# Optimization experiments

Measured on AMD Instinct MI355X. Metric: run time of the kernel, lower is better.

## Reference

```python
import jax, jax.numpy as jnp
import numpy as np

DIM = 1024
NUM_HEADS = 16
HEAD_DIM = DIM // NUM_HEADS

def setup_inputs() -> dict:
    key = jax.random.key(0)
    ks = jax.random.split(key, 5)
    s = 1.0 / np.sqrt(DIM)
    x = jax.random.normal(ks[0], (2, 2048, DIM), dtype=jnp.float32)
    W_qkv = jax.random.uniform(ks[1], (DIM, 3 * DIM), dtype=jnp.float32, minval=-s, maxval=s)
    b_qkv = jax.random.uniform(ks[2], (3 * DIM,), dtype=jnp.float32, minval=-s, maxval=s)
    W_out = jax.random.uniform(ks[3], (DIM, DIM), dtype=jnp.float32, minval=-s, maxval=s)
    b_out = jax.random.uniform(ks[4], (DIM,), dtype=jnp.float32, minval=-s, maxval=s)
    return {"x": x, "W_qkv": W_qkv, "b_qkv": b_qkv, "W_out": W_out, "b_out": b_out}

def reference(x, W_qkv, b_qkv, W_out, b_out):
    B, S, _ = x.shape
    qkv = x @ W_qkv + b_qkv                       # [B,S,3*dim]
    q, k, v = jnp.split(qkv, 3, axis=-1)
    # [B,S,dim] -> [B,H,S,hd]
    def to_heads(t):
        return t.reshape(B, S, NUM_HEADS, HEAD_DIM).transpose(0, 2, 1, 3)
    q, k, v = to_heads(q), to_heads(k), to_heads(v)
    scale = HEAD_DIM ** -0.5
    scores = jnp.einsum('bhqd,bhkd->bhqk', q, k) * scale
    attn = jax.nn.softmax(scores, axis=-1)
    out = jnp.einsum('bhqk,bhkd->bhqd', attn, v)  # [B,H,S,hd]
    out = out.transpose(0, 2, 1, 3).reshape(B, S, DIM)
    return out @ W_out + b_out
```

## Files before the change

### kernel.cpp

```cpp
#include <hip/hip_runtime.h>
#include <math.h>

#define DIMM    1024
#define NHEADS  16
#define HDIM    64
#define BATCH   2
#define SEQ     2048
#define ROWS    (BATCH*SEQ)

typedef _Float16 f16x8 __attribute__((ext_vector_type(8)));
typedef _Float16 f16x4 __attribute__((ext_vector_type(4)));
typedef float    f32x4 __attribute__((ext_vector_type(4)));
typedef float    f32x16 __attribute__((ext_vector_type(16)));

__device__ inline void gl_lds16(const void* g, void* l) {
    __builtin_amdgcn_global_load_lds(
        (const __attribute__((address_space(1))) void*)g,
        (__attribute__((address_space(3))) void*)l, 16, 0, 0);
}

static __device__ inline unsigned packh(_Float16 a, _Float16 b) {
    unsigned short ua = __builtin_bit_cast(unsigned short, a);
    unsigned short ub = __builtin_bit_cast(unsigned short, b);
    return (unsigned)ua | ((unsigned)ub << 16);
}
static __device__ inline f16x8 mkfrag(unsigned a, unsigned b, unsigned c, unsigned d) {
    union { unsigned u[4]; f16x8 v; } x;
    x.u[0] = a; x.u[1] = b; x.u[2] = c; x.u[3] = d;
    return x.v;
}

__device__ void tcvt64(const float* __restrict__ in, _Float16* __restrict__ out,
                       int K, int N, int k0, int n0, float (*tile)[65], int t)
{
    {
        const int c4 = (t & 15) * 4;
        const int r  = t >> 4;
        #pragma unroll
        for (int i = 0; i < 4; i++) {
            const int rr = r + 16 * i;
            float4 v = *(const float4*)(in + (size_t)(k0 + rr) * N + n0 + c4);
            tile[rr][c4] = v.x; tile[rr][c4 + 1] = v.y;
            tile[rr][c4 + 2] = v.z; tile[rr][c4 + 3] = v.w;
        }
    }
    __syncthreads();
    #pragma unroll
    for (int i = 0; i < 2; i++) {
        const int seg = t + 256 * i;
        const int n   = seg >> 3;
        const int kc  = (seg & 7) * 8;
        f16x8 o;
        #pragma unroll
        for (int j = 0; j < 8; j++) o[j] = (_Float16)tile[kc + j][n];
        *(f16x8*)(out + (size_t)(n0 + n) * K + k0 + kc) = o;
    }
}

__global__ __launch_bounds__(256)
void prep_kernel(const float* __restrict__ x, const float* __restrict__ Wqkv,
                 const float* __restrict__ Wout, _Float16* __restrict__ xh,
                 _Float16* __restrict__ wqkvt, _Float16* __restrict__ woutt)
{
    __shared__ float tile[64][65];
    const int bx = blockIdx.x;
    const int t  = threadIdx.x;
    if (bx < 2048) {
        const int i = bx * 256 + t;
        const float4 a = *(const float4*)(x + (size_t)i * 8);
        const float4 b = *(const float4*)(x + (size_t)i * 8 + 4);
        f16x8 o;
        o[0] = (_Float16)a.x; o[1] = (_Float16)a.y; o[2] = (_Float16)a.z; o[3] = (_Float16)a.w;
        o[4] = (_Float16)b.x; o[5] = (_Float16)b.y; o[6] = (_Float16)b.z; o[7] = (_Float16)b.w;
        *(f16x8*)(xh + (size_t)i * 8) = o;
    } else if (bx < 2816) {
        const int id = bx - 2048;
        const int gx = id % 48, gy = id / 48;
        tcvt64(Wqkv, wqkvt, DIMM, 3 * DIMM, gy * 64, gx * 64, tile, t);
    } else {
        const int id = bx - 2816;
        const int gx = id & 15, gy = id >> 4;
        tcvt64(Wout, woutt, DIMM, DIMM, gy * 64, gx * 64, tile, t);
    }
}

__global__ __launch_bounds__(256)
void vtranspose_kernel(const _Float16* __restrict__ qkvh, _Float16* __restrict__ vt)
{
    __shared__ _Float16 tile[64][72];
    const int kt = blockIdx.x;
    const int bh = blockIdx.y;
    const int b  = bh >> 4, h = bh & 15;
    const int t  = threadIdx.x;
    {
        const int key = t >> 2, c4 = (t & 3) * 16;
        const _Float16* src = qkvh + ((size_t)(b * SEQ + kt * 64 + key)) * (3 * DIMM)
                              + 2 * DIMM + h * HDIM + c4;
        f16x8 v0 = *(const f16x8*)src;
        f16x8 v1 = *(const f16x8*)(src + 8);
        #pragma unroll
        for (int j = 0; j < 8; j++) {
            tile[c4 + j][key]     = v0[j];
            tile[c4 + 8 + j][key] = v1[j];
        }
    }
    __syncthreads();
    {
        const int d = t >> 2, k4 = (t & 3) * 16;
        f16x8 o0, o1;
        #pragma unroll
        for (int j = 0; j < 8; j++) { o0[j] = tile[d][k4 + j]; o1[j] = tile[d][k4 + 8 + j]; }
        _Float16* dst = vt + ((size_t)bh * 64 + d) * SEQ + kt * 64 + k4;
        *(f16x8*)dst       = o0;
        *(f16x8*)(dst + 8) = o1;
    }
}

template<int OUT_F16, int BM>
__global__ __launch_bounds__(256)
void hgemm_db_kernel(const _Float16* __restrict__ A, const _Float16* __restrict__ Bt,
                     const float* __restrict__ bias, void* __restrict__ Cout,
                     int N, int K)
{
    constexpr int MI = BM / 32;
    __shared__ _Float16 As[2][BM * 64];
    __shared__ _Float16 Bs[2][128 * 64];

    const int t    = threadIdx.x;
    const int w    = t >> 6, lane = t & 63;
    const int quad = lane >> 4, l16 = lane & 15;
    const int wr   = w >> 1, wc = w & 1;
    const int row0 = blockIdx.y * BM, col0 = blockIdx.x * 128;
    const int sw   = l16 & 7;

    f32x4 acc[MI][4];
    #pragma unroll
    for (int i = 0; i < MI; i++)
        #pragma unroll
        for (int j = 0; j < 4; j++)
            #pragma unroll
            for (int r = 0; r < 4; r++) acc[i][j][r] = 0.f;

    const _Float16* gA[MI];
    int aofs[MI];
    #pragma unroll
    for (int j = 0; j < MI; j++) {
        const int s   = t + 256 * j;
        const int row = s >> 3;
        const int kb  = (s & 7) ^ (row & 7);
        gA[j] = A + (size_t)(row0 + row) * K + kb * 8;
        aofs[j] = s * 8;
    }
    const _Float16* gB[4];
    int bofs[4];
    #pragma unroll
    for (int j = 0; j < 4; j++) {
        const int s   = t + 256 * j;
        const int row = s >> 3;
        const int kb  = (s & 7) ^ (row & 7);
        gB[j] = Bt + (size_t)(col0 + row) * K + kb * 8;
        bofs[j] = s * 8;
    }

    #pragma unroll
    for (int j = 0; j < MI; j++) gl_lds16(gA[j], &As[0][aofs[j]]);
    #pragma unroll
    for (int j = 0; j < 4; j++)  gl_lds16(gB[j], &Bs[0][bofs[j]]);
    #pragma unroll
    for (int j = 0; j < MI; j++) gA[j] += 64;
    #pragma unroll
    for (int j = 0; j < 4; j++)  gB[j] += 64;

    const int niter = K >> 6;
    #pragma unroll 1
    for (int it = 0; it < niter; it++) {
        const int cur = it & 1;
        __syncthreads();

        if (it + 1 < niter) {
            const int nxt = cur ^ 1;
            #pragma unroll
            for (int j = 0; j < MI; j++) gl_lds16(gA[j], &As[nxt][aofs[j]]);
            #pragma unroll
            for (int j = 0; j < 4; j++)  gl_lds16(gB[j], &Bs[nxt][bofs[j]]);
            #pragma unroll
            for (int j = 0; j < MI; j++) gA[j] += 64;
            #pragma unroll
            for (int j = 0; j < 4; j++)  gB[j] += 64;
        }

        const _Float16* AsC = &As[cur][0];
        const _Float16* BsC = &Bs[cur][0];
        f16x8 af[MI][2], bf[4][2];
        #pragma unroll
        for (int i = 0; i < MI; i++) {
            const int arow = wr * (BM / 2) + i * 16 + l16;
            #pragma unroll
            for (int hh = 0; hh < 2; hh++)
                af[i][hh] = *(const f16x8*)(AsC + (arow * 8 + ((hh * 4 + quad) ^ sw)) * 8);
        }
        #pragma unroll
        for (int j = 0; j < 4; j++) {
            const int brow = wc * 64 + j * 16 + l16;
            #pragma unroll
            for (int hh = 0; hh < 2; hh++)
                bf[j][hh] = *(const f16x8*)(BsC + (brow * 8 + ((hh * 4 + quad) ^ sw)) * 8);
        }
        #pragma unroll
        for (int i = 0; i < MI; i++)
            #pragma unroll
            for (int j = 0; j < 4; j++) {
                acc[i][j] = __builtin_amdgcn_mfma_f32_16x16x32_f16(af[i][0], bf[j][0], acc[i][j], 0, 0, 0);
                acc[i][j] = __builtin_amdgcn_mfma_f32_16x16x32_f16(af[i][1], bf[j][1], acc[i][j], 0, 0, 0);
            }
    }

    #pragma unroll
    for (int j = 0; j < 4; j++) {
        const int col = col0 + wc * 64 + j * 16 + l16;
        const float bv = bias[col];
        #pragma unroll
        for (int i = 0; i < MI; i++) {
            const int row = row0 + wr * (BM / 2) + i * 16 + quad * 4;
            #pragma unroll
            for (int r = 0; r < 4; r++) {
                const float v = acc[i][j][r] + bv;
                if (OUT_F16)
                    ((_Float16*)Cout)[(size_t)(row + r) * N + col] = (_Float16)v;
                else
                    ((float*)Cout)[(size_t)(row + r) * N + col] = v;
            }
        }
    }
}

__global__ __launch_bounds__(256, 4)
void flash_attn_kernel(const _Float16* __restrict__ qkv,
                       const _Float16* __restrict__ vtg,
                       _Float16* __restrict__ out)
{
    const int qt = blockIdx.x;
    const int bh = blockIdx.y;
    const int b  = bh >> 4, hd = bh & 15;
    const int t    = threadIdx.x;
    const int w    = t >> 6;
    const int lane = t & 63;
    const int qg   = w >> 1;
    const int kh   = w & 1;
    const int l31  = lane & 31;
    const int hf   = lane >> 5;
    const int l7   = lane & 7;

    __shared__ __align__(16) _Float16 Ks [2][64 * 64];
    __shared__ __align__(16) _Float16 Vts[2][64 * 64];

    const int q0 = qt * 64;
    const size_t rstr = 3 * DIMM;
    const _Float16* qbase = qkv + (size_t)b * SEQ * rstr;

    f16x8 qf[4];
    {
        const _Float16* qrow = qbase + (size_t)(q0 + qg * 32 + l31) * rstr + hd * HDIM;
        #pragma unroll
        for (int dd = 0; dd < 4; dd++)
            qf[dd] = *(const f16x8*)(qrow + dd * 16 + hf * 8);
    }

    f32x16 Oacc[2];
    #pragma unroll
    for (int dh = 0; dh < 2; dh++)
        #pragma unroll
        for (int r = 0; r < 16; r++) Oacc[dh][r] = 0.f;
    float lrow = 0.f;

    const int seg0 = t, seg1 = t + 256;
    const int r0 = seg0 >> 3, lb0 = (seg0 & 7) ^ (r0 & 7);
    const int r1 = seg1 >> 3, lb1 = (seg1 & 7) ^ (r1 & 7);
    const _Float16* gK0 = qbase + (size_t)r0 * rstr + DIMM + hd * HDIM + lb0 * 8;
    const _Float16* gK1 = qbase + (size_t)r1 * rstr + DIMM + hd * HDIM + lb1 * 8;
    const _Float16* gV0 = vtg + ((size_t)bh * 64 + r0) * SEQ + lb0 * 8;
    const _Float16* gV1 = vtg + ((size_t)bh * 64 + r1) * SEQ + lb1 * 8;

    gl_lds16(gK0, &Ks [0][seg0 * 8]);
    gl_lds16(gK1, &Ks [0][seg1 * 8]);
    gl_lds16(gV0, &Vts[0][seg0 * 8]);
    gl_lds16(gV1, &Vts[0][seg1 * 8]);

    #pragma unroll 2
    for (int k0 = 0; k0 < SEQ; k0 += 64) {
        const int cur = (k0 >> 6) & 1;
        const _Float16* KsC  = &Ks [cur][0];
        const _Float16* VtsC = &Vts[cur][0];

        __syncthreads();

        f32x16 sacc;
        #pragma unroll
        for (int r = 0; r < 16; r++) sacc[r] = 0.f;
        #pragma unroll
        for (int dd = 0; dd < 4; dd++) {
            f16x8 kf = *(const f16x8*)(KsC + (kh * 32 + l31) * 64 + (((dd * 2 + hf) ^ l7) * 8));
            sacc = __builtin_amdgcn_mfma_f32_32x32x16_f16(kf, qf[dd], sacc, 0, 0, 0);
        }

        if (k0 + 64 < SEQ) {
            const int nxt = cur ^ 1;
            gl_lds16(gK0 + (size_t)(k0 + 64) * rstr, &Ks [nxt][seg0 * 8]);
            gl_lds16(gK1 + (size_t)(k0 + 64) * rstr, &Ks [nxt][seg1 * 8]);
            gl_lds16(gV0 + (k0 + 64),                &Vts[nxt][seg0 * 8]);
            gl_lds16(gV1 + (k0 + 64),                &Vts[nxt][seg1 * 8]);
        }

        _Float16 hh[16];
        #pragma unroll
        for (int r = 0; r < 16; r++) {
            const float e = __expf(sacc[r] * 0.125f);
            hh[r] = (_Float16)e;
            lrow += (float)hh[r];
        }

        unsigned w01 = packh(hh[0],  hh[1]),  w23 = packh(hh[2],  hh[3]);
        unsigned w45 = packh(hh[4],  hh[5]),  w67 = packh(hh[6],  hh[7]);
        unsigned w89 = packh(hh[8],  hh[9]),  wab = packh(hh[10], hh[11]);
        unsigned wcd = packh(hh[12], hh[13]), wef = packh(hh[14], hh[15]);
        unsigned o01 = __shfl_xor((int)w01, 32), o23 = __shfl_xor((int)w23, 32);
        unsigned o45 = __shfl_xor((int)w45, 32), o67 = __shfl_xor((int)w67, 32);
        unsigned o89 = __shfl_xor((int)w89, 32), oab = __shfl_xor((int)wab, 32);
        unsigned ocd = __shfl_xor((int)wcd, 32), oef = __shfl_xor((int)wef, 32);
        f16x8 pa0 = mkfrag(hf ? o45 : w01, hf ? o67 : w23,
                           hf ? w45 : o01, hf ? w67 : o23);
        f16x8 pa1 = mkfrag(hf ? ocd : w89, hf ? oef : wab,
                           hf ? wcd : o89, hf ? wef : oab);

        #pragma unroll
        for (int dh = 0; dh < 2; dh++) {
            const _Float16* vrow = VtsC + (dh * 32 + l31) * 64;
            f16x8 vf0 = *(const f16x8*)(vrow + (((kh * 4 + 0 + hf) ^ l7) * 8));
            f16x8 vf1 = *(const f16x8*)(vrow + (((kh * 4 + 2 + hf) ^ l7) * 8));
            Oacc[dh] = __builtin_amdgcn_mfma_f32_32x32x16_f16(pa0, vf0, Oacc[dh], 0, 0, 0);
            Oacc[dh] = __builtin_amdgcn_mfma_f32_32x32x16_f16(pa1, vf1, Oacc[dh], 0, 0, 0);
        }
    }

    float lsum = lrow + __shfl_xor(lrow, 32);
    __syncthreads();
    float* Obuf = (float*)&Ks[0][0];
    float* lbuf = (float*)&Vts[0][0];
    if (kh) {
        #pragma unroll
        for (int dh = 0; dh < 2; dh++)
            #pragma unroll
            for (int r = 0; r < 16; r++) {
                const int q = (r & 3) + 8 * (r >> 2) + 4 * hf;
                Obuf[(qg * 32 + q) * 64 + dh * 32 + l31] = Oacc[dh][r];
            }
        if (lane < 32) lbuf[qg * 32 + lane] = lsum;
    }
    __syncthreads();
    if (!kh) {
        const float dnrec = 1.f / (lsum + lbuf[qg * 32 + l31]);
        float dq[16];
        #pragma unroll
        for (int r = 0; r < 16; r++)
            dq[r] = __shfl(dnrec, (r & 3) + 8 * (r >> 2) + 4 * hf);
        #pragma unroll
        for (int dh = 0; dh < 2; dh++)
            #pragma unroll
            for (int r = 0; r < 16; r++) {
                const int q = (r & 3) + 8 * (r >> 2) + 4 * hf;
                const float v = (Oacc[dh][r] + Obuf[(qg * 32 + q) * 64 + dh * 32 + l31])
                                * dq[r];
                out[(size_t)(b * SEQ + q0 + qg * 32 + q) * DIMM + hd * HDIM + dh * 32 + l31] =
                    (_Float16)v;
            }
    }
}

extern "C" void kernel_launch(void* const* d_in, const int* in_sizes, int n_in,
                              void* d_out, int out_size, void* d_ws, size_t ws_size,
                              hipStream_t stream)
{
    const float* x    = (const float*)d_in[0];
    const float* Wqkv = (const float*)d_in[1];
    const float* bqkv = (const float*)d_in[2];
    const float* Wout = (const float*)d_in[3];
    const float* bout = (const float*)d_in[4];
    float* out = (float*)d_out;

    _Float16* qkvh  = (_Float16*)d_ws;
    _Float16* attnh = qkvh  + (size_t)ROWS * 3 * DIMM;
    _Float16* xh    = attnh + (size_t)ROWS * DIMM;
    _Float16* wqkvt = xh    + (size_t)ROWS * DIMM;
    _Float16* woutt = wqkvt + (size_t)3 * DIMM * DIMM;
    _Float16* vtg   = woutt + (size_t)DIMM * DIMM;

    prep_kernel<<<3072, 256, 0, stream>>>(x, Wqkv, Wout, xh, wqkvt, woutt);
    {
        dim3 grid(3 * DIMM / 128, ROWS / 128);
        hgemm_db_kernel<1, 128><<<grid, 256, 0, stream>>>(xh, wqkvt, bqkv, qkvh, 3 * DIMM, DIMM);
    }
    {
        dim3 grid(SEQ / 64, BATCH * NHEADS);
        vtranspose_kernel<<<grid, 256, 0, stream>>>(qkvh, vtg);
    }
    {
        dim3 grid(SEQ / 64, BATCH * NHEADS);
        flash_attn_kernel<<<grid, 256, 0, stream>>>(qkvh, vtg, attnh);
    }
    {
        dim3 grid(DIMM / 128, ROWS / 64);
        hgemm_db_kernel<0, 64><<<grid, 256, 0, stream>>>(attnh, woutt, bout, out, DIMM, DIMM);
    }
}
```

Before: 200.1 us.

## Fuse V transpose into QKV GEMM epilogue and use permlane32 swap for P

The QKV GEMM now writes the V columns directly in transposed [b,h,d,seq] layout from its epilogue, which removes the separate vtranspose kernel launch and its extra read and write of V. Separately, the flash-attention inner loop converts exp values with packed round-toward-zero conversion and rearranges halves with v_permlane32_swap instead of per-element shuffles. The row sum now accumulates the unrounded fp32 exponentials instead of the fp16-rounded values used in P. The transposed stores are 8-byte writes strided by SEQ, which coalesce less well than the GEMM's normal output path.

```diff
diff --git a/kernel.cpp b/kernel.cpp
--- a/kernel.cpp
+++ b/kernel.cpp
@@ -10,6 +10,7 @@
 
 typedef _Float16 f16x8 __attribute__((ext_vector_type(8)));
 typedef _Float16 f16x4 __attribute__((ext_vector_type(4)));
+typedef _Float16 f16x2 __attribute__((ext_vector_type(2)));
 typedef float    f32x4 __attribute__((ext_vector_type(4)));
 typedef float    f32x16 __attribute__((ext_vector_type(16)));
 
@@ -19,11 +20,6 @@
         (__attribute__((address_space(3))) void*)l, 16, 0, 0);
 }
 
-static __device__ inline unsigned packh(_Float16 a, _Float16 b) {
-    unsigned short ua = __builtin_bit_cast(unsigned short, a);
-    unsigned short ub = __builtin_bit_cast(unsigned short, b);
-    return (unsigned)ua | ((unsigned)ub << 16);
-}
 static __device__ inline f16x8 mkfrag(unsigned a, unsigned b, unsigned c, unsigned d) {
     union { unsigned u[4]; f16x8 v; } x;
     x.u[0] = a; x.u[1] = b; x.u[2] = c; x.u[3] = d;
@@ -84,43 +80,11 @@
     }
 }
 
-__global__ __launch_bounds__(256)
-void vtranspose_kernel(const _Float16* __restrict__ qkvh, _Float16* __restrict__ vt)
-{
-    __shared__ _Float16 tile[64][72];
-    const int kt = blockIdx.x;
-    const int bh = blockIdx.y;
-    const int b  = bh >> 4, h = bh & 15;
-    const int t  = threadIdx.x;
-    {
-        const int key = t >> 2, c4 = (t & 3) * 16;
-        const _Float16* src = qkvh + ((size_t)(b * SEQ + kt * 64 + key)) * (3 * DIMM)
-                              + 2 * DIMM + h * HDIM + c4;
-        f16x8 v0 = *(const f16x8*)src;
-        f16x8 v1 = *(const f16x8*)(src + 8);
-        #pragma unroll
-        for (int j = 0; j < 8; j++) {
-            tile[c4 + j][key]     = v0[j];
-            tile[c4 + 8 + j][key] = v1[j];
-        }
-    }
-    __syncthreads();
-    {
-        const int d = t >> 2, k4 = (t & 3) * 16;
-        f16x8 o0, o1;
-        #pragma unroll
-        for (int j = 0; j < 8; j++) { o0[j] = tile[d][k4 + j]; o1[j] = tile[d][k4 + 8 + j]; }
-        _Float16* dst = vt + ((size_t)bh * 64 + d) * SEQ + kt * 64 + k4;
-        *(f16x8*)dst       = o0;
-        *(f16x8*)(dst + 8) = o1;
-    }
-}
-
-template<int OUT_F16, int BM>
+template<int OUT_F16, int BM, int FUSEVT>
 __global__ __launch_bounds__(256)
 void hgemm_db_kernel(const _Float16* __restrict__ A, const _Float16* __restrict__ Bt,
                      const float* __restrict__ bias, void* __restrict__ Cout,
-                     int N, int K)
+                     _Float16* __restrict__ vtg, int N, int K)
 {
     constexpr int MI = BM / 32;
     __shared__ _Float16 As[2][BM * 64];
@@ -213,6 +177,27 @@
                 acc[i][j] = __builtin_amdgcn_mfma_f32_16x16x32_f16(af[i][0], bf[j][0], acc[i][j], 0, 0, 0);
                 acc[i][j] = __builtin_amdgcn_mfma_f32_16x16x32_f16(af[i][1], bf[j][1], acc[i][j], 0, 0, 0);
             }
+    }
+
+    if (FUSEVT && blockIdx.x >= 16) {
+        #pragma unroll
+        for (int j = 0; j < 4; j++) {
+            const int col = col0 + wc * 64 + j * 16 + l16;
+            const float bv = bias[col];
+            const int hv = (col - 2048) >> 6;
+            const int dv = col & 63;
+            #pragma unroll
+            for (int i = 0; i < MI; i++) {
+                const int row = row0 + wr * (BM / 2) + i * 16 + quad * 4;
+                const int bb  = row >> 11;
+                const int key = row & 2047;
+                f16x4 o;
+                #pragma unroll
+                for (int r = 0; r < 4; r++) o[r] = (_Float16)(acc[i][j][r] + bv);
+                *(f16x4*)(vtg + ((size_t)(bb * 16 + hv) * 64 + dv) * SEQ + key) = o;
+            }
+        }
+        return;
     }
 
     #pragma unroll
@@ -311,26 +296,31 @@
             gl_lds16(gV1 + (k0 + 64),                &Vts[nxt][seg1 * 8]);
         }
 
-        _Float16 hh[16];
+        float e[16];
         #pragma unroll
         for (int r = 0; r < 16; r++) {
-            const float e = __expf(sacc[r] * 0.125f);
-            hh[r] = (_Float16)e;
-            lrow += (float)hh[r];
-        }
-
-        unsigned w01 = packh(hh[0],  hh[1]),  w23 = packh(hh[2],  hh[3]);
-        unsigned w45 = packh(hh[4],  hh[5]),  w67 = packh(hh[6],  hh[7]);
-        unsigned w89 = packh(hh[8],  hh[9]),  wab = packh(hh[10], hh[11]);
-        unsigned wcd = packh(hh[12], hh[13]), wef = packh(hh[14], hh[15]);
-        unsigned o01 = __shfl_xor((int)w01, 32), o23 = __shfl_xor((int)w23, 32);
-        unsigned o45 = __shfl_xor((int)w45, 32), o67 = __shfl_xor((int)w67, 32);
-        unsigned o89 = __shfl_xor((int)w89, 32), oab = __shfl_xor((int)wab, 32);
-        unsigned ocd = __shfl_xor((int)wcd, 32), oef = __shfl_xor((int)wef, 32);
-        f16x8 pa0 = mkfrag(hf ? o45 : w01, hf ? o67 : w23,
-                           hf ? w45 : o01, hf ? w67 : o23);
-        f16x8 pa1 = mkfrag(hf ? ocd : w89, hf ? oef : wab,
-                           hf ? wcd : o89, hf ? wef : oab);
+            e[r] = __expf(sacc[r] * 0.125f);
+            lrow += e[r];
+        }
+
+        unsigned w01 = __builtin_bit_cast(unsigned, __builtin_amdgcn_cvt_pkrtz(e[0],  e[1]));
+        unsigned w23 = __builtin_bit_cast(unsigned, __builtin_amdgcn_cvt_pkrtz(e[2],  e[3]));
+        unsigned w45 = __builtin_bit_cast(unsigned, __builtin_amdgcn_cvt_pkrtz(e[4],  e[5]));
+        unsigned w67 = __builtin_bit_cast(unsigned, __builtin_amdgcn_cvt_pkrtz(e[6],  e[7]));
+        unsigned w89 = __builtin_bit_cast(unsigned, __builtin_amdgcn_cvt_pkrtz(e[8],  e[9]));
+        unsigned wab = __builtin_bit_cast(unsigned, __builtin_amdgcn_cvt_pkrtz(e[10], e[11]));
+        unsigned wcd = __builtin_bit_cast(unsigned, __builtin_amdgcn_cvt_pkrtz(e[12], e[13]));
+        unsigned wef = __builtin_bit_cast(unsigned, __builtin_amdgcn_cvt_pkrtz(e[14], e[15]));
+        unsigned p00 = w01, p02 = w45;
+        asm("v_permlane32_swap_b32 %0, %1" : "+v"(p00), "+v"(p02));
+        unsigned p01 = w23, p03 = w67;
+        asm("v_permlane32_swap_b32 %0, %1" : "+v"(p01), "+v"(p03));
+        unsigned p10 = w89, p12 = wcd;
+        asm("v_permlane32_swap_b32 %0, %1" : "+v"(p10), "+v"(p12));
+        unsigned p11 = wab, p13 = wef;
+        asm("v_permlane32_swap_b32 %0, %1" : "+v"(p11), "+v"(p13));
+        f16x8 pa0 = mkfrag(p00, p01, p02, p03);
+        f16x8 pa1 = mkfrag(p10, p11, p12, p13);
 
         #pragma unroll
         for (int dh = 0; dh < 2; dh++) {
@@ -397,11 +387,7 @@
     prep_kernel<<<3072, 256, 0, stream>>>(x, Wqkv, Wout, xh, wqkvt, woutt);
     {
         dim3 grid(3 * DIMM / 128, ROWS / 128);
-        hgemm_db_kernel<1, 128><<<grid, 256, 0, stream>>>(xh, wqkvt, bqkv, qkvh, 3 * DIMM, DIMM);
-    }
-    {
-        dim3 grid(SEQ / 64, BATCH * NHEADS);
-        vtranspose_kernel<<<grid, 256, 0, stream>>>(qkvh, vtg);
+        hgemm_db_kernel<1, 128, 1><<<grid, 256, 0, stream>>>(xh, wqkvt, bqkv, qkvh, vtg, 3 * DIMM, DIMM);
     }
     {
         dim3 grid(SEQ / 64, BATCH * NHEADS);
@@ -409,6 +395,6 @@
     }
     {
         dim3 grid(DIMM / 128, ROWS / 64);
-        hgemm_db_kernel<0, 64><<<grid, 256, 0, stream>>>(attnh, woutt, bout, out, DIMM, DIMM);
-    }
-}
+        hgemm_db_kernel<0, 64, 0><<<grid, 256, 0, stream>>>(attnh, woutt, bout, out, nullptr, DIMM, DIMM);
+    }
+}
```

Result: faster. 190.6 us (-4.7%).
